# Performance work log

Measured on AMD Instinct MI355X. Metric: run time of the kernel, lower is better.

## Reference

```python
import jax, jax.numpy as jnp
import numpy as np

N_NODES = 50000
N_EDGES = 640000
M_DIM = 128
D_DIM = 128
H_DIM = M_DIM // 2
NORM_EPS = 1e-5


def setup_inputs() -> dict:
    key = jax.random.key(0)
    ks = jax.random.split(key, 8)
    messages = jax.random.normal(ks[0], (N_EDGES, M_DIM), dtype=jnp.float32)
    target_indices = jax.random.randint(ks[1], (N_EDGES,), 0, N_NODES, dtype=jnp.int64)
    node_features = jax.random.normal(ks[2], (N_NODES, D_DIM), dtype=jnp.float32)
    # attention scorer params (torch Linear: weight [out,in])
    W1 = 0.02 * jax.random.normal(ks[3], (H_DIM, M_DIM + D_DIM), dtype=jnp.float32)
    b1 = jnp.zeros((H_DIM,), dtype=jnp.float32)
    W2 = 0.02 * jax.random.normal(ks[4], (1, H_DIM), dtype=jnp.float32)
    gamma = jnp.ones((M_DIM,), dtype=jnp.float32)
    beta = jnp.zeros((M_DIM,), dtype=jnp.float32)
    return {"messages": messages, "target_indices": target_indices,
            "node_features": node_features, "n_nodes": N_NODES,
            "W1": W1, "b1": b1, "W2": W2, "gamma": gamma, "beta": beta}


def reference(messages, target_indices, node_features, n_nodes, W1, b1, W2, gamma, beta):
    # gather target node feats per edge: [E, D]
    target_feats = node_features[target_indices]
    attn_input = jnp.concatenate([messages, target_feats], axis=-1)  # [E, M+D]
    h = jax.nn.gelu(attn_input @ W1.T + b1, approximate=False)       # [E, M//2]
    raw_scores = (h @ W2.T)[:, 0]                                    # [E]
    weights = jax.nn.sigmoid(raw_scores)                             # [E]
    weighted = messages * weights[:, None]                           # [E, M]
    aggregated = jax.ops.segment_sum(weighted, target_indices, num_segments=n_nodes)  # [N, M]
    sum_weights = jax.ops.segment_sum(weights, target_indices, num_segments=n_nodes)  # [N]
    aggregated = aggregated / (sum_weights[:, None] + 1e-8)
    # LayerNorm over last dim
    mu = jnp.mean(aggregated, axis=-1, keepdims=True)
    var = jnp.var(aggregated, axis=-1, keepdims=True)
    normed = (aggregated - mu) * jax.lax.rsqrt(var + NORM_EPS)
    return normed * gamma + beta
```

## Files before the change

### kernel.cpp

```cpp
#include <hip/hip_runtime.h>
#include <hip/hip_bf16.h>

#define EDGES   640000
#define NNODES  50000
#define MDIM    128
#define HDIM    64
#define XSTR    36

typedef __attribute__((ext_vector_type(8))) short bshort8;
typedef __attribute__((ext_vector_type(4))) float f32x4;

__device__ __forceinline__ short f2bf(float f) {
    __hip_bfloat16 h = __float2bfloat16(f);
    return *reinterpret_cast<short*>(&h);
}

__device__ __forceinline__ float gelu_fast(float h) {
    const float x  = h * 0.70710678118654752f;
    const float ax = fabsf(x);
    const float t  = __builtin_amdgcn_rcpf(fmaf(0.3275911f, ax, 1.0f));
    float p = fmaf(1.061405429f, t, -1.453152027f);
    p = fmaf(p, t,  1.421413741f);
    p = fmaf(p, t, -0.284496736f);
    p = fmaf(p, t,  0.254829592f);
    p *= t;
    const float e = __expf(-x * x);
    float er = fmaf(-p, e, 1.0f);
    er = (x < 0.0f) ? -er : er;
    return 0.5f * h * (1.0f + er);
}

__global__ void k0_prep(const float* __restrict__ w1,
                        short* __restrict__ bpack, float* __restrict__ w1dt) {
    const int i = blockIdx.x * 256 + threadIdx.x;
    if (i < 8192) {
        const int ii   = i & 7;
        const int lane = (i >> 3) & 63;
        const int jtkc = i >> 9;
        const int kc = jtkc >> 2, jt = jtkc & 3;
        const int j = jt * 16 + (lane & 15);
        const int k = kc * 32 + (lane >> 4) * 8 + ii;
        bpack[i] = f2bf(w1[j * 256 + k]);
    } else if (i < 16384) {
        const int t = i - 8192;
        const int k = t >> 6, j = t & 63;
        w1dt[t] = w1[j * 256 + 128 + k];
    }
}

__global__ __launch_bounds__(256, 4) void kg_nodes(
    const float* __restrict__ feats, const float* __restrict__ w1dt,
    const float* __restrict__ b1, float* __restrict__ g)
{
    __shared__ float xs[4][64 * XSTR];
    const int wv = threadIdx.x >> 6, L = threadIdx.x & 63;
    const long base = ((long)blockIdx.x * 4 + wv) * 64;
    float* xb = xs[wv];
    float h[HDIM];
#pragma unroll
    for (int j = 0; j < HDIM; ++j) h[j] = 0.0f;
    const int gq = L >> 3, sub = L & 7;
    for (int c = 0; c < 4; ++c) {
        const int col0 = c * 32;
#pragma unroll
        for (int r = 0; r < 8; ++r) {
            long row = base + gq + 8 * r;
            if (row > NNODES - 1) row = NNODES - 1;
            float4 v = *(const float4*)(feats + row * MDIM + col0 + sub * 4);
            *(float4*)(xb + (gq + 8 * r) * XSTR + sub * 4) = v;
        }
        __syncthreads();
        for (int k4 = 0; k4 < 8; ++k4) {
            const float4 xv = *(const float4*)(xb + L * XSTR + 4 * k4);
            const float* colw = w1dt + (c * 32 + 4 * k4) * HDIM;
            const float xa[4] = {xv.x, xv.y, xv.z, xv.w};
#pragma unroll
            for (int kk = 0; kk < 4; ++kk) {
                const float xk = xa[kk];
#pragma unroll
                for (int j = 0; j < HDIM; ++j)
                    h[j] = fmaf(colw[kk * HDIM + j], xk, h[j]);
            }
        }
        __syncthreads();
    }
    const long row = base + L;
    if (row < NNODES) {
        float* gp = g + row * HDIM;
#pragma unroll
        for (int j4 = 0; j4 < 16; ++j4) {
            float4 b4 = *(const float4*)(b1 + 4 * j4);
            float4 o;
            o.x = h[4 * j4 + 0] + b4.x; o.y = h[4 * j4 + 1] + b4.y;
            o.z = h[4 * j4 + 2] + b4.z; o.w = h[4 * j4 + 3] + b4.w;
            *(float4*)(gp + 4 * j4) = o;
        }
    }
}

__global__ __launch_bounds__(256) void k1_weights(
    const float* __restrict__ msgs, const int* __restrict__ tgt,
    const short* __restrict__ bpack, const float* __restrict__ g,
    const float* __restrict__ w2, float* __restrict__ weights,
    int* __restrict__ counts)
{
    const int wv = threadIdx.x >> 6, L = threadIdx.x & 63;
    const long base = ((long)blockIdx.x * 4 + wv) * 16;
    const int n = L & 15, quad = L >> 4;
    const bshort8* bp = (const bshort8*)bpack;

    const float* rp = msgs + (base + n) * MDIM + quad * 8;
    float4 v[8];
#pragma unroll
    for (int kc = 0; kc < 4; ++kc) {
        v[2 * kc]     = *(const float4*)(rp + kc * 32);
        v[2 * kc + 1] = *(const float4*)(rp + kc * 32 + 4);
    }

    float w2v[4];
#pragma unroll
    for (int jt = 0; jt < 4; ++jt) w2v[jt] = w2[jt * 16 + n];

    f32x4 hacc[4];
#pragma unroll
    for (int jt = 0; jt < 4; ++jt) hacc[jt] = (f32x4){0.f, 0.f, 0.f, 0.f};
#pragma unroll
    for (int kc = 0; kc < 4; ++kc) {
        const float4 va = v[2 * kc], vb = v[2 * kc + 1];
        bshort8 a;
        a[0] = f2bf(va.x); a[1] = f2bf(va.y); a[2] = f2bf(va.z); a[3] = f2bf(va.w);
        a[4] = f2bf(vb.x); a[5] = f2bf(vb.y); a[6] = f2bf(vb.z); a[7] = f2bf(vb.w);
#pragma unroll
        for (int jt = 0; jt < 4; ++jt)
            hacc[jt] = __builtin_amdgcn_mfma_f32_16x16x32_bf16(a, bp[(kc * 4 + jt) * 64 + L], hacc[jt], 0, 0, 0);
    }

#pragma unroll
    for (int r = 0; r < 4; ++r) {
        const long e = base + quad * 4 + r;
        const int t = tgt[e];
        const float* gp = g + (long)t * HDIM;
        float raw = 0.0f;
#pragma unroll
        for (int jt = 0; jt < 4; ++jt) {
            const float hj = hacc[jt][r] + gp[jt * 16 + n];
            raw = fmaf(gelu_fast(hj), w2v[jt], raw);
        }
#pragma unroll
        for (int off = 1; off < 16; off <<= 1)
            raw += __shfl_xor(raw, off, 64);
        if (n == r) {
            weights[e] = 1.0f / (1.0f + __expf(-raw));
            atomicAdd(&counts[t], 1);
        }
    }
}

__global__ void kscan_local(const int* __restrict__ counts, int* __restrict__ offsets,
                            int* __restrict__ blocksums) {
    __shared__ int s[256];
    const int tid = threadIdx.x;
    const int i = blockIdx.x * 256 + tid;
    int v = (i < NNODES) ? counts[i] : 0;
    s[tid] = v;
    __syncthreads();
    for (int d = 1; d < 256; d <<= 1) {
        int t = (tid >= d) ? s[tid - d] : 0;
        __syncthreads();
        s[tid] += t;
        __syncthreads();
    }
    if (i < NNODES) offsets[i] = s[tid];
    if (tid == 255) blocksums[blockIdx.x] = s[255];
}

__global__ void kscan_blk(int* __restrict__ blocksums, int nblk) {
    __shared__ int s[256];
    const int tid = threadIdx.x;
    int v = (tid < nblk) ? blocksums[tid] : 0;
    s[tid] = v;
    __syncthreads();
    for (int d = 1; d < 256; d <<= 1) {
        int t = (tid >= d) ? s[tid - d] : 0;
        __syncthreads();
        s[tid] += t;
        __syncthreads();
    }
    if (tid < nblk) blocksums[tid] = s[tid] - v;
}

__global__ void kscan_fix(int* __restrict__ offsets, const int* __restrict__ blocksums,
                          const int* __restrict__ counts, int* __restrict__ cursor) {
    const int i = blockIdx.x * 256 + threadIdx.x;
    if (i < NNODES) {
        const int incl = offsets[i] + blocksums[i >> 8];
        offsets[i] = incl;
        cursor[i] = incl - counts[i];
    }
}

__global__ void kscatter(const int* __restrict__ tgt, int* __restrict__ cursor,
                         int* __restrict__ eidx) {
    const int e = blockIdx.x * 256 + threadIdx.x;
    if (e < EDGES) {
        const int pos = atomicAdd(&cursor[tgt[e]], 1);
        eidx[pos] = e;
    }
}

__global__ __launch_bounds__(256) void kagg(
    const float* __restrict__ msgs, const float* __restrict__ wts,
    const int* __restrict__ eidx, const int* __restrict__ offsets,
    const float* __restrict__ gamma, const float* __restrict__ beta,
    float* __restrict__ out)
{
    const int L = threadIdx.x & 63, wv = threadIdx.x >> 6;
    const int node = blockIdx.x * 4 + wv;
    if (node >= NNODES) return;
    const int end = offsets[node];
    const int beg = (node == 0) ? 0 : offsets[node - 1];

    const int c0 = 4 * (L & 31);
    const int half = L >> 5;
    float4 acc = {0.0f, 0.0f, 0.0f, 0.0f};
    float swl = 0.0f;

    for (int b = beg; b < end; b += 64) {
        int m = end - b; if (m > 64) m = 64;
        int eid = 0; float w = 0.0f;
        if (L < m) { eid = eidx[b + L]; w = wts[eid]; }
        swl += w;
        const int nit = (m + 1) >> 1;
        for (int i = 0; i < nit; ++i) {
            const int   e0 = __shfl(eid, 2 * i, 64);
            const int   e1 = __shfl(eid, 2 * i + 1, 64);
            const float w0 = __shfl(w,   2 * i, 64);
            const float w1 = __shfl(w,   2 * i + 1, 64);
            const int   er = half ? e1 : e0;
            const float wr = half ? w1 : w0;
            const float4 mv = *(const float4*)(msgs + (long)er * MDIM + c0);
            acc.x = fmaf(mv.x, wr, acc.x);
            acc.y = fmaf(mv.y, wr, acc.y);
            acc.z = fmaf(mv.z, wr, acc.z);
            acc.w = fmaf(mv.w, wr, acc.w);
        }
    }

    acc.x += __shfl_xor(acc.x, 32, 64);
    acc.y += __shfl_xor(acc.y, 32, 64);
    acc.z += __shfl_xor(acc.z, 32, 64);
    acc.w += __shfl_xor(acc.w, 32, 64);

    float s1 = acc.x + acc.y + acc.z + acc.w;
    float s2 = acc.x * acc.x + acc.y * acc.y + acc.z * acc.z + acc.w * acc.w;
#pragma unroll
    for (int off = 16; off; off >>= 1) {
        s1 += __shfl_xor(s1, off, 64);
        s2 += __shfl_xor(s2, off, 64);
    }
#pragma unroll
    for (int off = 32; off; off >>= 1)
        swl += __shfl_xor(swl, off, 64);

    const float inv = 1.0f / (swl + 1e-8f);
    const float mu = s1 * inv * (1.0f / MDIM);
    const float var = s2 * inv * inv * (1.0f / MDIM) - mu * mu;
    const float rs = rsqrtf(var + 1e-5f);

    if (half == 0) {
        const float4 gm = *(const float4*)(gamma + c0);
        const float4 bt = *(const float4*)(beta + c0);
        float4 o;
        o.x = (acc.x * inv - mu) * rs * gm.x + bt.x;
        o.y = (acc.y * inv - mu) * rs * gm.y + bt.y;
        o.z = (acc.z * inv - mu) * rs * gm.z + bt.z;
        o.w = (acc.w * inv - mu) * rs * gm.w + bt.w;
        *(float4*)(out + (long)node * MDIM + c0) = o;
    }
}

extern "C" void kernel_launch(void* const* d_in, const int* in_sizes, int n_in,
                              void* d_out, int out_size, void* d_ws, size_t ws_size,
                              hipStream_t stream) {
    const float* msgs  = (const float*)d_in[0];
    const int*   tgt   = (const int*)d_in[1];
    const float* feats = (const float*)d_in[2];
    const float* W1    = (const float*)d_in[4];
    const float* b1    = (const float*)d_in[5];
    const float* W2    = (const float*)d_in[6];
    const float* gamma = (const float*)d_in[7];
    const float* beta  = (const float*)d_in[8];
    float* out = (float*)d_out;

    char* ws = (char*)d_ws;
    short* bpack   = (short*)(ws + 0);
    float* w1dt    = (float*)(ws + (32 << 10));
    int*   counts  = (int*)  (ws + (64 << 10));
    int*   offsets = (int*)  (ws + (320 << 10));
    int*   cursor  = (int*)  (ws + (576 << 10));
    int*   bsums   = (int*)  (ws + (832 << 10));
    float* wts     = (float*)(ws + (1 << 20));
    int*   eidx    = (int*)  (ws + (4 << 20));
    float* g       = (float*)(ws + (8 << 20));

    hipMemsetAsync(counts, 0, NNODES * sizeof(int), stream);

    k0_prep<<<64, 256, 0, stream>>>(W1, bpack, w1dt);
    kg_nodes<<<(NNODES + 255) / 256, 256, 0, stream>>>(feats, w1dt, b1, g);
    k1_weights<<<EDGES / 64, 256, 0, stream>>>(msgs, tgt, bpack, g, W2, wts, counts);
    const int nblk = (NNODES + 255) / 256;
    kscan_local<<<nblk, 256, 0, stream>>>(counts, offsets, bsums);
    kscan_blk<<<1, 256, 0, stream>>>(bsums, nblk);
    kscan_fix<<<nblk, 256, 0, stream>>>(offsets, bsums, counts, cursor);
    kscatter<<<(EDGES + 255) / 256, 256, 0, stream>>>(tgt, cursor, eidx);
    kagg<<<(NNODES + 3) / 4, 256, 0, stream>>>(msgs, wts, eidx, offsets, gamma, beta, out);
}
```

Before: 632.3 us.

## Process eight edges per iteration in aggregation; vectorize G and W2 loads

The aggregation kernel now gives each group of 8 lanes one edge row, with each lane loading 16 floats. That puts 8 edges in flight per iteration instead of 2, which should expose more memory-level parallelism for the gathered message rows. The partial sums are combined with a transpose-style butterfly of shuffles so each lane ends up owning two output columns, and the LayerNorm reduction loops are merged. In the edge-score kernel, the packed W1 columns are permuted so each lane's four hidden units are contiguous, which turns the per-node g lookups and the W2 loads into single float4 loads. The cost is more registers and extra shuffle work during the reduction.

After: 632.6 us. Within noise of the previous version (+0.1%).

```diff
diff --git a/kernel.cpp b/kernel.cpp
--- a/kernel.cpp
+++ b/kernel.cpp
@@ -38,7 +38,7 @@
         const int lane = (i >> 3) & 63;
         const int jtkc = i >> 9;
         const int kc = jtkc >> 2, jt = jtkc & 3;
-        const int j = jt * 16 + (lane & 15);
+        const int j = 4 * (lane & 15) + jt;
         const int k = kc * 32 + (lane >> 4) * 8 + ii;
         bpack[i] = f2bf(w1[j * 256 + k]);
     } else if (i < 16384) {
@@ -117,9 +117,7 @@
         v[2 * kc + 1] = *(const float4*)(rp + kc * 32 + 4);
     }
 
-    float w2v[4];
-#pragma unroll
-    for (int jt = 0; jt < 4; ++jt) w2v[jt] = w2[jt * 16 + n];
+    const float4 w2v = *(const float4*)(w2 + 4 * n);
 
     f32x4 hacc[4];
 #pragma unroll
@@ -139,12 +137,17 @@
     for (int r = 0; r < 4; ++r) {
         const long e = base + quad * 4 + r;
         const int t = tgt[e];
-        const float* gp = g + (long)t * HDIM;
-        float raw = 0.0f;
-#pragma unroll
-        for (int jt = 0; jt < 4; ++jt) {
-            const float hj = hacc[jt][r] + gp[jt * 16 + n];
-            raw = fmaf(gelu_fast(hj), w2v[jt], raw);
+        const float4 g4 = *(const float4*)(g + (long)t * HDIM + 4 * n);
+        float raw;
+        {
+            const float h0 = hacc[0][r] + g4.x;
+            const float h1 = hacc[1][r] + g4.y;
+            const float h2 = hacc[2][r] + g4.z;
+            const float h3 = hacc[3][r] + g4.w;
+            raw = gelu_fast(h0) * w2v.x;
+            raw = fmaf(gelu_fast(h1), w2v.y, raw);
+            raw = fmaf(gelu_fast(h2), w2v.z, raw);
+            raw = fmaf(gelu_fast(h3), w2v.w, raw);
         }
 #pragma unroll
         for (int off = 1; off < 16; off <<= 1)
@@ -219,64 +222,92 @@
     if (node >= NNODES) return;
     const int end = offsets[node];
     const int beg = (node == 0) ? 0 : offsets[node - 1];
-
-    const int c0 = 4 * (L & 31);
-    const int half = L >> 5;
-    float4 acc = {0.0f, 0.0f, 0.0f, 0.0f};
+    const int m = end - beg;
+
+    const int gr = L >> 3;
+    const int lg = L & 7;
+    float4 a0 = {0.f,0.f,0.f,0.f}, a1 = a0, a2 = a0, a3 = a0;
     float swl = 0.0f;
 
-    for (int b = beg; b < end; b += 64) {
-        int m = end - b; if (m > 64) m = 64;
+    for (int b = 0; b < m; b += 64) {
+        int mm = m - b; if (mm > 64) mm = 64;
         int eid = 0; float w = 0.0f;
-        if (L < m) { eid = eidx[b + L]; w = wts[eid]; }
+        if (L < mm) { eid = eidx[beg + b + L]; w = wts[eid]; }
         swl += w;
-        const int nit = (m + 1) >> 1;
+        const int nit = (mm + 7) >> 3;
         for (int i = 0; i < nit; ++i) {
-            const int   e0 = __shfl(eid, 2 * i, 64);
-            const int   e1 = __shfl(eid, 2 * i + 1, 64);
-            const float w0 = __shfl(w,   2 * i, 64);
-            const float w1 = __shfl(w,   2 * i + 1, 64);
-            const int   er = half ? e1 : e0;
-            const float wr = half ? w1 : w0;
-            const float4 mv = *(const float4*)(msgs + (long)er * MDIM + c0);
-            acc.x = fmaf(mv.x, wr, acc.x);
-            acc.y = fmaf(mv.y, wr, acc.y);
-            acc.z = fmaf(mv.z, wr, acc.z);
-            acc.w = fmaf(mv.w, wr, acc.w);
-        }
-    }
-
-    acc.x += __shfl_xor(acc.x, 32, 64);
-    acc.y += __shfl_xor(acc.y, 32, 64);
-    acc.z += __shfl_xor(acc.z, 32, 64);
-    acc.w += __shfl_xor(acc.w, 32, 64);
-
-    float s1 = acc.x + acc.y + acc.z + acc.w;
-    float s2 = acc.x * acc.x + acc.y * acc.y + acc.z * acc.z + acc.w * acc.w;
-#pragma unroll
-    for (int off = 16; off; off >>= 1) {
+            const int slot = i * 8 + gr;
+            const int   er = __shfl(eid, slot, 64);
+            const float wr = __shfl(w,   slot, 64);
+            const float* rp = msgs + (long)er * MDIM + lg * 16;
+            const float4 v0 = *(const float4*)(rp);
+            const float4 v1 = *(const float4*)(rp + 4);
+            const float4 v2 = *(const float4*)(rp + 8);
+            const float4 v3 = *(const float4*)(rp + 12);
+            a0.x = fmaf(v0.x, wr, a0.x); a0.y = fmaf(v0.y, wr, a0.y);
+            a0.z = fmaf(v0.z, wr, a0.z); a0.w = fmaf(v0.w, wr, a0.w);
+            a1.x = fmaf(v1.x, wr, a1.x); a1.y = fmaf(v1.y, wr, a1.y);
+            a1.z = fmaf(v1.z, wr, a1.z); a1.w = fmaf(v1.w, wr, a1.w);
+            a2.x = fmaf(v2.x, wr, a2.x); a2.y = fmaf(v2.y, wr, a2.y);
+            a2.z = fmaf(v2.z, wr, a2.z); a2.w = fmaf(v2.w, wr, a2.w);
+            a3.x = fmaf(v3.x, wr, a3.x); a3.y = fmaf(v3.y, wr, a3.y);
+            a3.z = fmaf(v3.z, wr, a3.z); a3.w = fmaf(v3.w, wr, a3.w);
+        }
+    }
+
+    {
+        const float4 k0 = (gr & 1) ? a2 : a0;
+        const float4 k1 = (gr & 1) ? a3 : a1;
+        const float4 s0 = (gr & 1) ? a0 : a2;
+        const float4 s1 = (gr & 1) ? a1 : a3;
+        a0.x = k0.x + __shfl_xor(s0.x, 8, 64);
+        a0.y = k0.y + __shfl_xor(s0.y, 8, 64);
+        a0.z = k0.z + __shfl_xor(s0.z, 8, 64);
+        a0.w = k0.w + __shfl_xor(s0.w, 8, 64);
+        a1.x = k1.x + __shfl_xor(s1.x, 8, 64);
+        a1.y = k1.y + __shfl_xor(s1.y, 8, 64);
+        a1.z = k1.z + __shfl_xor(s1.z, 8, 64);
+        a1.w = k1.w + __shfl_xor(s1.w, 8, 64);
+    }
+    {
+        const float4 k0 = (gr & 2) ? a1 : a0;
+        const float4 s0 = (gr & 2) ? a0 : a1;
+        a0.x = k0.x + __shfl_xor(s0.x, 16, 64);
+        a0.y = k0.y + __shfl_xor(s0.y, 16, 64);
+        a0.z = k0.z + __shfl_xor(s0.z, 16, 64);
+        a0.w = k0.w + __shfl_xor(s0.w, 16, 64);
+    }
+    float S0, S1;
+    {
+        const float kx = (gr & 4) ? a0.z : a0.x;
+        const float ky = (gr & 4) ? a0.w : a0.y;
+        const float sx = (gr & 4) ? a0.x : a0.z;
+        const float sy = (gr & 4) ? a0.y : a0.w;
+        S0 = kx + __shfl_xor(sx, 32, 64);
+        S1 = ky + __shfl_xor(sy, 32, 64);
+    }
+    const int col = lg * 16 + (gr & 1) * 8 + ((gr & 2) << 1) + ((gr & 4) >> 1);
+
+    float s1 = S0 + S1;
+    float s2 = S0 * S0 + S1 * S1;
+#pragma unroll
+    for (int off = 32; off; off >>= 1) {
         s1 += __shfl_xor(s1, off, 64);
         s2 += __shfl_xor(s2, off, 64);
-    }
-#pragma unroll
-    for (int off = 32; off; off >>= 1)
         swl += __shfl_xor(swl, off, 64);
+    }
 
     const float inv = 1.0f / (swl + 1e-8f);
+    const float a0v = S0 * inv, a1v = S1 * inv;
     const float mu = s1 * inv * (1.0f / MDIM);
     const float var = s2 * inv * inv * (1.0f / MDIM) - mu * mu;
     const float rs = rsqrtf(var + 1e-5f);
-
-    if (half == 0) {
-        const float4 gm = *(const float4*)(gamma + c0);
-        const float4 bt = *(const float4*)(beta + c0);
-        float4 o;
-        o.x = (acc.x * inv - mu) * rs * gm.x + bt.x;
-        o.y = (acc.y * inv - mu) * rs * gm.y + bt.y;
-        o.z = (acc.z * inv - mu) * rs * gm.z + bt.z;
-        o.w = (acc.w * inv - mu) * rs * gm.w + bt.w;
-        *(float4*)(out + (long)node * MDIM + c0) = o;
-    }
+    const float2 gm = *(const float2*)(gamma + col);
+    const float2 bt = *(const float2*)(beta + col);
+    float2 o;
+    o.x = (a0v - mu) * rs * gm.x + bt.x;
+    o.y = (a1v - mu) * rs * gm.y + bt.y;
+    *(float2*)(out + (long)node * MDIM + col) = o;
 }
 
 extern "C" void kernel_launch(void* const* d_in, const int* in_sizes, int n_in,
```
